# Optimization experiments

Measured on AMD Instinct MI355X. Metric: run time of the kernel, lower is better.

The kernel has to match this reference:

```python
import jax, jax.numpy as jnp
import numpy as np

D = 4096

def setup_inputs() -> dict:
    key = jax.random.key(0)
    ks = jax.random.split(key, 14)
    s = 1.0 / np.sqrt(D)
    return {
        "x": jax.random.normal(ks[0], (D,), jnp.float32),
        "state_xx": jax.random.normal(ks[1], (D,), jnp.float32),
        "aa": jax.random.normal(ks[2], (D,), jnp.float32),
        "bb": jax.random.uniform(ks[3], (D,), jnp.float32) + 0.5,  # positive running denom
        "pp": jax.random.normal(ks[4], (D,), jnp.float32),
        "w_key": jax.random.normal(ks[5], (D, D), jnp.float32) * s,
        "w_val": jax.random.normal(ks[6], (D, D), jnp.float32) * s,
        "w_rec": jax.random.normal(ks[7], (D, D), jnp.float32) * s,
        "w_out": jax.random.normal(ks[8], (D, D), jnp.float32) * s,
        "t_decay": -jax.random.uniform(ks[9], (D,), jnp.float32),  # module stores -exp(time_decay) < 0
        "t_first": jax.random.normal(ks[10], (D,), jnp.float32) * 0.5,
        "t_mix_k": jax.random.uniform(ks[11], (D,), jnp.float32),
        "t_mix_v": jax.random.uniform(ks[12], (D,), jnp.float32),
        "t_mix_r": jax.random.uniform(ks[13], (D,), jnp.float32),
    }


def reference(x, state_xx, aa, bb, pp, w_key, w_val, w_rec, w_out,
              t_decay, t_first, t_mix_k, t_mix_v, t_mix_r):
    # token mixing with previous token (state_xx)
    xk = x * t_mix_k + state_xx * (1.0 - t_mix_k)
    xv = x * t_mix_v + state_xx * (1.0 - t_mix_v)
    xr = x * t_mix_r + state_xx * (1.0 - t_mix_r)

    r = jax.nn.sigmoid(w_rec @ xr)
    k = w_key @ xk
    v = w_val @ xv

    # stabilized WKV output using current token bonus t_first
    ww = t_first + k
    p = jnp.maximum(pp, ww)
    e1 = jnp.exp(pp - p)
    e2 = jnp.exp(ww - p)
    a = e1 * aa + e2 * v
    b = e1 * bb + e2

    # stabilized state update with decay
    ww2 = pp + t_decay
    p2 = jnp.maximum(ww2, k)
    e1b = jnp.exp(ww2 - p2)
    e2b = jnp.exp(k - p2)
    new_aa = e1b * aa + e2b * v
    new_bb = e1b * bb + e2b
    new_pp = p2

    y = w_out @ (r * (a / b))
    # (output, new state_xx, new aa, new bb, new pp)
    return (y, x, new_aa, new_bb, new_pp)
```

## Files before the change

### kernel.cpp

```cpp
#include <hip/hip_runtime.h>

#define DIM 4096
#define BLK 256

__global__ void __launch_bounds__(BLK) vecprep_kernel(
    const float* __restrict__ x, const float* __restrict__ sxx,
    const float* __restrict__ tmk, const float* __restrict__ tmv,
    const float* __restrict__ tmr,
    float* __restrict__ xk, float* __restrict__ xv, float* __restrict__ xr) {
  int i = blockIdx.x * BLK + threadIdx.x;
  float xi = x[i], si = sxx[i];
  float mk = tmk[i], mv = tmv[i], mr = tmr[i];
  xk[i] = xi * mk + si * (1.0f - mk);
  xv[i] = xi * mv + si * (1.0f - mv);
  xr[i] = xi * mr + si * (1.0f - mr);
}

__global__ void __launch_bounds__(BLK) matvec3_kernel(
    const float* __restrict__ wr, const float* __restrict__ wk,
    const float* __restrict__ wv,
    const float* __restrict__ xr, const float* __restrict__ xk,
    const float* __restrict__ xv,
    float* __restrict__ rr, float* __restrict__ k, float* __restrict__ v) {
  const int row = blockIdx.x;
  const int t = threadIdx.x;
  const float4* wr4 = (const float4*)(wr + (size_t)row * DIM);
  const float4* wk4 = (const float4*)(wk + (size_t)row * DIM);
  const float4* wv4 = (const float4*)(wv + (size_t)row * DIM);
  const float4* xr4 = (const float4*)xr;
  const float4* xk4 = (const float4*)xk;
  const float4* xv4 = (const float4*)xv;
  float sr = 0.f, sk = 0.f, sv = 0.f;
#pragma unroll
  for (int j = 0; j < DIM / 4 / BLK; ++j) {
    int idx = t + j * BLK;
    float4 a = wr4[idx]; float4 b = xr4[idx];
    sr += a.x * b.x + a.y * b.y + a.z * b.z + a.w * b.w;
    float4 c = wk4[idx]; float4 d = xk4[idx];
    sk += c.x * d.x + c.y * d.y + c.z * d.z + c.w * d.w;
    float4 e = wv4[idx]; float4 f = xv4[idx];
    sv += e.x * f.x + e.y * f.y + e.z * f.z + e.w * f.w;
  }
  for (int off = 32; off > 0; off >>= 1) {
    sr += __shfl_down(sr, off);
    sk += __shfl_down(sk, off);
    sv += __shfl_down(sv, off);
  }
  __shared__ float red[4][3];
  int wave = t >> 6, lane = t & 63;
  if (lane == 0) { red[wave][0] = sr; red[wave][1] = sk; red[wave][2] = sv; }
  __syncthreads();
  if (t == 0) {
    float a = 0.f, b = 0.f, c = 0.f;
    for (int w = 0; w < 4; ++w) { a += red[w][0]; b += red[w][1]; c += red[w][2]; }
    rr[row] = a; k[row] = b; v[row] = c;
  }
}

__global__ void __launch_bounds__(BLK) wkv_kernel(
    const float* __restrict__ x, const float* __restrict__ aa,
    const float* __restrict__ bb, const float* __restrict__ pp,
    const float* __restrict__ t_decay, const float* __restrict__ t_first,
    const float* __restrict__ k, const float* __restrict__ v,
    const float* __restrict__ rr,
    float* __restrict__ rab, float* __restrict__ out_x,
    float* __restrict__ out_aa, float* __restrict__ out_bb,
    float* __restrict__ out_pp) {
  int i = blockIdx.x * BLK + threadIdx.x;
  float kk = k[i], vv = v[i];
  float r = 1.0f / (1.0f + expf(-rr[i]));
  float ppi = pp[i], aai = aa[i], bbi = bb[i];
  float ww = t_first[i] + kk;
  float p = fmaxf(ppi, ww);
  float e1 = expf(ppi - p), e2 = expf(ww - p);
  float a = e1 * aai + e2 * vv;
  float b = e1 * bbi + e2;
  rab[i] = r * (a / b);
  float ww2 = ppi + t_decay[i];
  float p2 = fmaxf(ww2, kk);
  float e1b = expf(ww2 - p2), e2b = expf(kk - p2);
  out_x[i] = x[i];
  out_aa[i] = e1b * aai + e2b * vv;
  out_bb[i] = e1b * bbi + e2b;
  out_pp[i] = p2;
}

__global__ void __launch_bounds__(BLK) matvec1_kernel(
    const float* __restrict__ w, const float* __restrict__ xin,
    float* __restrict__ y) {
  const int row = blockIdx.x;
  const int t = threadIdx.x;
  const float4* w4 = (const float4*)(w + (size_t)row * DIM);
  const float4* x4 = (const float4*)xin;
  float s = 0.f;
#pragma unroll
  for (int j = 0; j < DIM / 4 / BLK; ++j) {
    int idx = t + j * BLK;
    float4 a = w4[idx]; float4 b = x4[idx];
    s += a.x * b.x + a.y * b.y + a.z * b.z + a.w * b.w;
  }
  for (int off = 32; off > 0; off >>= 1) s += __shfl_down(s, off);
  __shared__ float red[4];
  int wave = t >> 6, lane = t & 63;
  if (lane == 0) red[wave] = s;
  __syncthreads();
  if (t == 0) y[row] = red[0] + red[1] + red[2] + red[3];
}

extern "C" void kernel_launch(void* const* d_in, const int* in_sizes, int n_in,
                              void* d_out, int out_size, void* d_ws, size_t ws_size,
                              hipStream_t stream) {
  const float* x       = (const float*)d_in[0];
  const float* sxx     = (const float*)d_in[1];
  const float* aa      = (const float*)d_in[2];
  const float* bb      = (const float*)d_in[3];
  const float* pp      = (const float*)d_in[4];
  const float* w_key   = (const float*)d_in[5];
  const float* w_val   = (const float*)d_in[6];
  const float* w_rec   = (const float*)d_in[7];
  const float* w_out   = (const float*)d_in[8];
  const float* t_decay = (const float*)d_in[9];
  const float* t_first = (const float*)d_in[10];
  const float* t_mix_k = (const float*)d_in[11];
  const float* t_mix_v = (const float*)d_in[12];
  const float* t_mix_r = (const float*)d_in[13];

  float* out    = (float*)d_out;
  float* y      = out;
  float* out_x  = out + DIM;
  float* out_aa = out + 2 * DIM;
  float* out_bb = out + 3 * DIM;
  float* out_pp = out + 4 * DIM;

  float* ws  = (float*)d_ws;
  float* xk  = ws;
  float* xv  = ws + DIM;
  float* xr  = ws + 2 * DIM;
  float* k   = ws + 3 * DIM;
  float* v   = ws + 4 * DIM;
  float* rr  = ws + 5 * DIM;
  float* rab = ws + 6 * DIM;

  vecprep_kernel<<<DIM / BLK, BLK, 0, stream>>>(x, sxx, t_mix_k, t_mix_v, t_mix_r,
                                                xk, xv, xr);
  matvec3_kernel<<<DIM, BLK, 0, stream>>>(w_rec, w_key, w_val, xr, xk, xv,
                                          rr, k, v);
  wkv_kernel<<<DIM / BLK, BLK, 0, stream>>>(x, aa, bb, pp, t_decay, t_first,
                                            k, v, rr, rab, out_x, out_aa,
                                            out_bb, out_pp);
  matvec1_kernel<<<DIM, BLK, 0, stream>>>(w_out, rab, y);
}
```

Baseline: 262.9 us.

## Fuse token mix and WKV into matvec, process four rows per block

Computes the token-mixed vectors inside the first matvec kernel and applies the WKV update in its epilogue, removing two kernel launches and the intermediate workspace traffic. Each block now processes four rows, so the input vector loads are reused across rows and more weight loads are in flight per thread. In exchange, each block recomputes the mixing of the full vector and register pressure goes up.

```diff
diff --git a/kernel.cpp b/kernel.cpp
--- a/kernel.cpp
+++ b/kernel.cpp
@@ -2,109 +2,152 @@
 
 #define DIM 4096
 #define BLK 256
+#define ROWS 4
 
-__global__ void __launch_bounds__(BLK) vecprep_kernel(
+__device__ __forceinline__ float dot4(float4 a, float4 b) {
+  return a.x * b.x + a.y * b.y + a.z * b.z + a.w * b.w;
+}
+
+__device__ __forceinline__ float4 mix4(float4 xi, float4 si, float4 m) {
+  float4 r;
+  r.x = fmaf(xi.x - si.x, m.x, si.x);
+  r.y = fmaf(xi.y - si.y, m.y, si.y);
+  r.z = fmaf(xi.z - si.z, m.z, si.z);
+  r.w = fmaf(xi.w - si.w, m.w, si.w);
+  return r;
+}
+
+__global__ void __launch_bounds__(BLK) fused3_kernel(
     const float* __restrict__ x, const float* __restrict__ sxx,
     const float* __restrict__ tmk, const float* __restrict__ tmv,
     const float* __restrict__ tmr,
-    float* __restrict__ xk, float* __restrict__ xv, float* __restrict__ xr) {
-  int i = blockIdx.x * BLK + threadIdx.x;
-  float xi = x[i], si = sxx[i];
-  float mk = tmk[i], mv = tmv[i], mr = tmr[i];
-  xk[i] = xi * mk + si * (1.0f - mk);
-  xv[i] = xi * mv + si * (1.0f - mv);
-  xr[i] = xi * mr + si * (1.0f - mr);
-}
-
-__global__ void __launch_bounds__(BLK) matvec3_kernel(
     const float* __restrict__ wr, const float* __restrict__ wk,
     const float* __restrict__ wv,
-    const float* __restrict__ xr, const float* __restrict__ xk,
-    const float* __restrict__ xv,
-    float* __restrict__ rr, float* __restrict__ k, float* __restrict__ v) {
-  const int row = blockIdx.x;
+    const float* __restrict__ aa, const float* __restrict__ bb,
+    const float* __restrict__ pp,
+    const float* __restrict__ t_decay, const float* __restrict__ t_first,
+    float* __restrict__ rab, float* __restrict__ out_x,
+    float* __restrict__ out_aa, float* __restrict__ out_bb,
+    float* __restrict__ out_pp) {
   const int t = threadIdx.x;
-  const float4* wr4 = (const float4*)(wr + (size_t)row * DIM);
-  const float4* wk4 = (const float4*)(wk + (size_t)row * DIM);
-  const float4* wv4 = (const float4*)(wv + (size_t)row * DIM);
-  const float4* xr4 = (const float4*)xr;
-  const float4* xk4 = (const float4*)xk;
-  const float4* xv4 = (const float4*)xv;
-  float sr = 0.f, sk = 0.f, sv = 0.f;
+  const int row0 = blockIdx.x * ROWS;
+
+  const float4* x4 = (const float4*)x;
+  const float4* s4 = (const float4*)sxx;
+  const float4* mk4 = (const float4*)tmk;
+  const float4* mv4 = (const float4*)tmv;
+  const float4* mr4 = (const float4*)tmr;
+
+  float4 fxr[4], fxk[4], fxv[4];
 #pragma unroll
-  for (int j = 0; j < DIM / 4 / BLK; ++j) {
+  for (int j = 0; j < 4; ++j) {
     int idx = t + j * BLK;
-    float4 a = wr4[idx]; float4 b = xr4[idx];
-    sr += a.x * b.x + a.y * b.y + a.z * b.z + a.w * b.w;
-    float4 c = wk4[idx]; float4 d = xk4[idx];
-    sk += c.x * d.x + c.y * d.y + c.z * d.z + c.w * d.w;
-    float4 e = wv4[idx]; float4 f = xv4[idx];
-    sv += e.x * f.x + e.y * f.y + e.z * f.z + e.w * f.w;
+    float4 xi = x4[idx], si = s4[idx];
+    fxk[j] = mix4(xi, si, mk4[idx]);
+    fxv[j] = mix4(xi, si, mv4[idx]);
+    fxr[j] = mix4(xi, si, mr4[idx]);
   }
+
+  float accr[ROWS], acck[ROWS], accv[ROWS];
+#pragma unroll
+  for (int r = 0; r < ROWS; ++r) { accr[r] = acck[r] = accv[r] = 0.f; }
+
+#pragma unroll
+  for (int r = 0; r < ROWS; ++r) {
+    const float4* wrp = (const float4*)(wr + (size_t)(row0 + r) * DIM);
+    const float4* wkp = (const float4*)(wk + (size_t)(row0 + r) * DIM);
+    const float4* wvp = (const float4*)(wv + (size_t)(row0 + r) * DIM);
+#pragma unroll
+    for (int j = 0; j < 4; ++j) {
+      int idx = t + j * BLK;
+      accr[r] += dot4(wrp[idx], fxr[j]);
+      acck[r] += dot4(wkp[idx], fxk[j]);
+      accv[r] += dot4(wvp[idx], fxv[j]);
+    }
+  }
+
+#pragma unroll
   for (int off = 32; off > 0; off >>= 1) {
-    sr += __shfl_down(sr, off);
-    sk += __shfl_down(sk, off);
-    sv += __shfl_down(sv, off);
+#pragma unroll
+    for (int r = 0; r < ROWS; ++r) {
+      accr[r] += __shfl_down(accr[r], off);
+      acck[r] += __shfl_down(acck[r], off);
+      accv[r] += __shfl_down(accv[r], off);
+    }
   }
-  __shared__ float red[4][3];
-  int wave = t >> 6, lane = t & 63;
-  if (lane == 0) { red[wave][0] = sr; red[wave][1] = sk; red[wave][2] = sv; }
+  __shared__ float red[4][ROWS * 3];
+  const int wave = t >> 6, lane = t & 63;
+  if (lane == 0) {
+#pragma unroll
+    for (int r = 0; r < ROWS; ++r) {
+      red[wave][r * 3 + 0] = accr[r];
+      red[wave][r * 3 + 1] = acck[r];
+      red[wave][r * 3 + 2] = accv[r];
+    }
+  }
   __syncthreads();
-  if (t == 0) {
-    float a = 0.f, b = 0.f, c = 0.f;
-    for (int w = 0; w < 4; ++w) { a += red[w][0]; b += red[w][1]; c += red[w][2]; }
-    rr[row] = a; k[row] = b; v[row] = c;
+
+  if (t < ROWS) {
+    const int row = row0 + t;
+    float sr = red[0][t * 3 + 0] + red[1][t * 3 + 0] + red[2][t * 3 + 0] + red[3][t * 3 + 0];
+    float sk = red[0][t * 3 + 1] + red[1][t * 3 + 1] + red[2][t * 3 + 1] + red[3][t * 3 + 1];
+    float sv = red[0][t * 3 + 2] + red[1][t * 3 + 2] + red[2][t * 3 + 2] + red[3][t * 3 + 2];
+
+    float rsig = 1.0f / (1.0f + expf(-sr));
+    float ppi = pp[row], aai = aa[row], bbi = bb[row];
+    float ww = t_first[row] + sk;
+    float p = fmaxf(ppi, ww);
+    float e1 = expf(ppi - p), e2 = expf(ww - p);
+    float a = e1 * aai + e2 * sv;
+    float b = e1 * bbi + e2;
+    rab[row] = rsig * (a / b);
+    float ww2 = ppi + t_decay[row];
+    float p2 = fmaxf(ww2, sk);
+    float e1b = expf(ww2 - p2), e2b = expf(sk - p2);
+    out_x[row]  = x[row];
+    out_aa[row] = e1b * aai + e2b * sv;
+    out_bb[row] = e1b * bbi + e2b;
+    out_pp[row] = p2;
   }
 }
 
-__global__ void __launch_bounds__(BLK) wkv_kernel(
-    const float* __restrict__ x, const float* __restrict__ aa,
-    const float* __restrict__ bb, const float* __restrict__ pp,
-    const float* __restrict__ t_decay, const float* __restrict__ t_first,
-    const float* __restrict__ k, const float* __restrict__ v,
-    const float* __restrict__ rr,
-    float* __restrict__ rab, float* __restrict__ out_x,
-    float* __restrict__ out_aa, float* __restrict__ out_bb,
-    float* __restrict__ out_pp) {
-  int i = blockIdx.x * BLK + threadIdx.x;
-  float kk = k[i], vv = v[i];
-  float r = 1.0f / (1.0f + expf(-rr[i]));
-  float ppi = pp[i], aai = aa[i], bbi = bb[i];
-  float ww = t_first[i] + kk;
-  float p = fmaxf(ppi, ww);
-  float e1 = expf(ppi - p), e2 = expf(ww - p);
-  float a = e1 * aai + e2 * vv;
-  float b = e1 * bbi + e2;
-  rab[i] = r * (a / b);
-  float ww2 = ppi + t_decay[i];
-  float p2 = fmaxf(ww2, kk);
-  float e1b = expf(ww2 - p2), e2b = expf(kk - p2);
-  out_x[i] = x[i];
-  out_aa[i] = e1b * aai + e2b * vv;
-  out_bb[i] = e1b * bbi + e2b;
-  out_pp[i] = p2;
-}
-
-__global__ void __launch_bounds__(BLK) matvec1_kernel(
+__global__ void __launch_bounds__(BLK) matvec_out_kernel(
     const float* __restrict__ w, const float* __restrict__ xin,
     float* __restrict__ y) {
-  const int row = blockIdx.x;
   const int t = threadIdx.x;
-  const float4* w4 = (const float4*)(w + (size_t)row * DIM);
+  const int row0 = blockIdx.x * ROWS;
   const float4* x4 = (const float4*)xin;
-  float s = 0.f;
+
+  float4 fx[4];
 #pragma unroll
-  for (int j = 0; j < DIM / 4 / BLK; ++j) {
-    int idx = t + j * BLK;
-    float4 a = w4[idx]; float4 b = x4[idx];
-    s += a.x * b.x + a.y * b.y + a.z * b.z + a.w * b.w;
+  for (int j = 0; j < 4; ++j) fx[j] = x4[t + j * BLK];
+
+  float acc[ROWS];
+#pragma unroll
+  for (int r = 0; r < ROWS; ++r) acc[r] = 0.f;
+
+#pragma unroll
+  for (int r = 0; r < ROWS; ++r) {
+    const float4* wp = (const float4*)(w + (size_t)(row0 + r) * DIM);
+#pragma unroll
+    for (int j = 0; j < 4; ++j) acc[r] += dot4(wp[t + j * BLK], fx[j]);
   }
-  for (int off = 32; off > 0; off >>= 1) s += __shfl_down(s, off);
-  __shared__ float red[4];
-  int wave = t >> 6, lane = t & 63;
-  if (lane == 0) red[wave] = s;
+
+#pragma unroll
+  for (int off = 32; off > 0; off >>= 1) {
+#pragma unroll
+    for (int r = 0; r < ROWS; ++r) acc[r] += __shfl_down(acc[r], off);
+  }
+  __shared__ float red[4][ROWS];
+  const int wave = t >> 6, lane = t & 63;
+  if (lane == 0) {
+#pragma unroll
+    for (int r = 0; r < ROWS; ++r) red[wave][r] = acc[r];
+  }
   __syncthreads();
-  if (t == 0) y[row] = red[0] + red[1] + red[2] + red[3];
+  if (t < ROWS) {
+    y[row0 + t] = red[0][t] + red[1][t] + red[2][t] + red[3][t];
+  }
 }
 
 extern "C" void kernel_launch(void* const* d_in, const int* in_sizes, int n_in,
@@ -132,21 +175,11 @@
   float* out_bb = out + 3 * DIM;
   float* out_pp = out + 4 * DIM;
 
-  float* ws  = (float*)d_ws;
-  float* xk  = ws;
-  float* xv  = ws + DIM;
-  float* xr  = ws + 2 * DIM;
-  float* k   = ws + 3 * DIM;
-  float* v   = ws + 4 * DIM;
-  float* rr  = ws + 5 * DIM;
-  float* rab = ws + 6 * DIM;
+  float* rab = (float*)d_ws;
 
-  vecprep_kernel<<<DIM / BLK, BLK, 0, stream>>>(x, sxx, t_mix_k, t_mix_v, t_mix_r,
-                                                xk, xv, xr);
-  matvec3_kernel<<<DIM, BLK, 0, stream>>>(w_rec, w_key, w_val, xr, xk, xv,
-                                          rr, k, v);
-  wkv_kernel<<<DIM / BLK, BLK, 0, stream>>>(x, aa, bb, pp, t_decay, t_first,
-                                            k, v, rr, rab, out_x, out_aa,
-                                            out_bb, out_pp);
-  matvec1_kernel<<<DIM, BLK, 0, stream>>>(w_out, rab, y);
+  fused3_kernel<<<DIM / ROWS, BLK, 0, stream>>>(
+      x, sxx, t_mix_k, t_mix_v, t_mix_r, w_rec, w_key, w_val,
+      aa, bb, pp, t_decay, t_first,
+      rab, out_x, out_aa, out_bb, out_pp);
+  matvec_out_kernel<<<DIM / ROWS, BLK, 0, stream>>>(w_out, rab, y);
 }
```

Result: no change. 258.9 us (-1.5%).

## Split matvec rows across waves with atomic accumulation and float4 prep

Applied to the files above, without the earlier changes.

Each matvec row is now split into four column chunks, each handled by one wave. A wave computes two rows, 2048 apart, and adds its partial sum to the output with atomicAdd, so block-level shared-memory reduction and __syncthreads are no longer needed. The prep kernel is vectorised to float4 and also zeroes the k, v, rr and y accumulators before the atomics run. The aim is to cut block reduction overhead and hold the x-vector slices in registers, at the cost of atomic traffic and summation order that is no longer deterministic.

```diff
diff --git a/kernel.cpp b/kernel.cpp
--- a/kernel.cpp
+++ b/kernel.cpp
@@ -3,57 +3,82 @@
 #define DIM 4096
 #define BLK 256
 
-__global__ void __launch_bounds__(BLK) vecprep_kernel(
+__device__ __forceinline__ float dot4(float4 a, float4 b) {
+  return a.x * b.x + a.y * b.y + a.z * b.z + a.w * b.w;
+}
+
+__device__ __forceinline__ float wave_reduce(float s) {
+#pragma unroll
+  for (int off = 32; off > 0; off >>= 1) s += __shfl_down(s, off);
+  return s;
+}
+
+__global__ void __launch_bounds__(BLK) prep_kernel(
     const float* __restrict__ x, const float* __restrict__ sxx,
     const float* __restrict__ tmk, const float* __restrict__ tmv,
     const float* __restrict__ tmr,
-    float* __restrict__ xk, float* __restrict__ xv, float* __restrict__ xr) {
+    float* __restrict__ xk, float* __restrict__ xv, float* __restrict__ xr,
+    float* __restrict__ k, float* __restrict__ v, float* __restrict__ rr,
+    float* __restrict__ y) {
   int i = blockIdx.x * BLK + threadIdx.x;
-  float xi = x[i], si = sxx[i];
-  float mk = tmk[i], mv = tmv[i], mr = tmr[i];
-  xk[i] = xi * mk + si * (1.0f - mk);
-  xv[i] = xi * mv + si * (1.0f - mv);
-  xr[i] = xi * mr + si * (1.0f - mr);
+  const float4* x4 = (const float4*)x;
+  const float4* s4 = (const float4*)sxx;
+  const float4* mk4 = (const float4*)tmk;
+  const float4* mv4 = (const float4*)tmv;
+  const float4* mr4 = (const float4*)tmr;
+  float4 xi = x4[i], si = s4[i];
+  float4 mk = mk4[i], mv = mv4[i], mr = mr4[i];
+  float4 ok, ov, orr;
+  ok.x = fmaf(xi.x - si.x, mk.x, si.x); ok.y = fmaf(xi.y - si.y, mk.y, si.y);
+  ok.z = fmaf(xi.z - si.z, mk.z, si.z); ok.w = fmaf(xi.w - si.w, mk.w, si.w);
+  ov.x = fmaf(xi.x - si.x, mv.x, si.x); ov.y = fmaf(xi.y - si.y, mv.y, si.y);
+  ov.z = fmaf(xi.z - si.z, mv.z, si.z); ov.w = fmaf(xi.w - si.w, mv.w, si.w);
+  orr.x = fmaf(xi.x - si.x, mr.x, si.x); orr.y = fmaf(xi.y - si.y, mr.y, si.y);
+  orr.z = fmaf(xi.z - si.z, mr.z, si.z); orr.w = fmaf(xi.w - si.w, mr.w, si.w);
+  ((float4*)xk)[i] = ok;
+  ((float4*)xv)[i] = ov;
+  ((float4*)xr)[i] = orr;
+  float4 z = make_float4(0.f, 0.f, 0.f, 0.f);
+  ((float4*)k)[i] = z;
+  ((float4*)v)[i] = z;
+  ((float4*)rr)[i] = z;
+  ((float4*)y)[i] = z;
 }
 
-__global__ void __launch_bounds__(BLK) matvec3_kernel(
+__global__ void __launch_bounds__(BLK) matvec3_split(
     const float* __restrict__ wr, const float* __restrict__ wk,
     const float* __restrict__ wv,
     const float* __restrict__ xr, const float* __restrict__ xk,
     const float* __restrict__ xv,
     float* __restrict__ rr, float* __restrict__ k, float* __restrict__ v) {
-  const int row = blockIdx.x;
-  const int t = threadIdx.x;
-  const float4* wr4 = (const float4*)(wr + (size_t)row * DIM);
-  const float4* wk4 = (const float4*)(wk + (size_t)row * DIM);
-  const float4* wv4 = (const float4*)(wv + (size_t)row * DIM);
-  const float4* xr4 = (const float4*)xr;
-  const float4* xk4 = (const float4*)xk;
-  const float4* xv4 = (const float4*)xv;
-  float sr = 0.f, sk = 0.f, sv = 0.f;
+  const int lane = threadIdx.x & 63;
+  const int wid = blockIdx.x * (BLK / 64) + (threadIdx.x >> 6);
+  const int c = wid & 3;
+  const int r0 = wid >> 2;
+  const int col = c * 256 + lane;
+
+  const float4* wmat[3] = {(const float4*)wr, (const float4*)wk, (const float4*)wv};
+  const float4* xvec[3] = {(const float4*)xr, (const float4*)xk, (const float4*)xv};
+  float* ovec[3] = {rr, k, v};
+
 #pragma unroll
-  for (int j = 0; j < DIM / 4 / BLK; ++j) {
-    int idx = t + j * BLK;
-    float4 a = wr4[idx]; float4 b = xr4[idx];
-    sr += a.x * b.x + a.y * b.y + a.z * b.z + a.w * b.w;
-    float4 c = wk4[idx]; float4 d = xk4[idx];
-    sk += c.x * d.x + c.y * d.y + c.z * d.z + c.w * d.w;
-    float4 e = wv4[idx]; float4 f = xv4[idx];
-    sv += e.x * f.x + e.y * f.y + e.z * f.z + e.w * f.w;
-  }
-  for (int off = 32; off > 0; off >>= 1) {
-    sr += __shfl_down(sr, off);
-    sk += __shfl_down(sk, off);
-    sv += __shfl_down(sv, off);
-  }
-  __shared__ float red[4][3];
-  int wave = t >> 6, lane = t & 63;
-  if (lane == 0) { red[wave][0] = sr; red[wave][1] = sk; red[wave][2] = sv; }
-  __syncthreads();
-  if (t == 0) {
-    float a = 0.f, b = 0.f, c = 0.f;
-    for (int w = 0; w < 4; ++w) { a += red[w][0]; b += red[w][1]; c += red[w][2]; }
-    rr[row] = a; k[row] = b; v[row] = c;
+  for (int m = 0; m < 3; ++m) {
+    const float4* xp = xvec[m];
+    float4 xf0 = xp[col];
+    float4 xf1 = xp[col + 64];
+    float4 xf2 = xp[col + 128];
+    float4 xf3 = xp[col + 192];
+#pragma unroll
+    for (int h = 0; h < 2; ++h) {
+      const int r = r0 + h * 2048;
+      const float4* wrow = wmat[m] + (size_t)r * 1024 + col;
+      float s = dot4(wrow[0], xf0);
+      s += dot4(wrow[64], xf1);
+      s += dot4(wrow[128], xf2);
+      s += dot4(wrow[192], xf3);
+      s = wave_reduce(s);
+      if (lane == 0) atomicAdd(ovec[m] + r, s);
+    }
   }
 }
 
@@ -85,26 +110,31 @@
   out_pp[i] = p2;
 }
 
-__global__ void __launch_bounds__(BLK) matvec1_kernel(
+__global__ void __launch_bounds__(BLK) matvec_out_split(
     const float* __restrict__ w, const float* __restrict__ xin,
     float* __restrict__ y) {
-  const int row = blockIdx.x;
-  const int t = threadIdx.x;
-  const float4* w4 = (const float4*)(w + (size_t)row * DIM);
-  const float4* x4 = (const float4*)xin;
-  float s = 0.f;
+  const int lane = threadIdx.x & 63;
+  const int wid = blockIdx.x * (BLK / 64) + (threadIdx.x >> 6);
+  const int c = wid & 3;
+  const int r0 = wid >> 2;
+  const int col = c * 256 + lane;
+
+  const float4* xp = (const float4*)xin;
+  float4 xf0 = xp[col];
+  float4 xf1 = xp[col + 64];
+  float4 xf2 = xp[col + 128];
+  float4 xf3 = xp[col + 192];
 #pragma unroll
-  for (int j = 0; j < DIM / 4 / BLK; ++j) {
-    int idx = t + j * BLK;
-    float4 a = w4[idx]; float4 b = x4[idx];
-    s += a.x * b.x + a.y * b.y + a.z * b.z + a.w * b.w;
+  for (int h = 0; h < 2; ++h) {
+    const int r = r0 + h * 2048;
+    const float4* wrow = (const float4*)w + (size_t)r * 1024 + col;
+    float s = dot4(wrow[0], xf0);
+    s += dot4(wrow[64], xf1);
+    s += dot4(wrow[128], xf2);
+    s += dot4(wrow[192], xf3);
+    s = wave_reduce(s);
+    if (lane == 0) atomicAdd(y + r, s);
   }
-  for (int off = 32; off > 0; off >>= 1) s += __shfl_down(s, off);
-  __shared__ float red[4];
-  int wave = t >> 6, lane = t & 63;
-  if (lane == 0) red[wave] = s;
-  __syncthreads();
-  if (t == 0) y[row] = red[0] + red[1] + red[2] + red[3];
 }
 
 extern "C" void kernel_launch(void* const* d_in, const int* in_sizes, int n_in,
@@ -141,12 +171,12 @@
   float* rr  = ws + 5 * DIM;
   float* rab = ws + 6 * DIM;
 
-  vecprep_kernel<<<DIM / BLK, BLK, 0, stream>>>(x, sxx, t_mix_k, t_mix_v, t_mix_r,
-                                                xk, xv, xr);
-  matvec3_kernel<<<DIM, BLK, 0, stream>>>(w_rec, w_key, w_val, xr, xk, xv,
+  prep_kernel<<<DIM / 4 / BLK, BLK, 0, stream>>>(
+      x, sxx, t_mix_k, t_mix_v, t_mix_r, xk, xv, xr, k, v, rr, y);
+  matvec3_split<<<2048, BLK, 0, stream>>>(w_rec, w_key, w_val, xr, xk, xv,
                                           rr, k, v);
   wkv_kernel<<<DIM / BLK, BLK, 0, stream>>>(x, aa, bb, pp, t_decay, t_first,
                                             k, v, rr, rab, out_x, out_aa,
                                             out_bb, out_pp);
-  matvec1_kernel<<<DIM, BLK, 0, stream>>>(w_out, rab, y);
+  matvec_out_split<<<2048, BLK, 0, stream>>>(w_out, rab, y);
 }
```

Measured after the change: 260.7 us. About the same (-0.8%).

## Fuse token-mix into matvec, use wave-per-row blocks with shared input vector

Applied to the files above, without the earlier changes.

The separate vecprep kernel is removed, and each block of the three-matrix matvec now computes its mixed input vector into shared memory directly. Both matvec kernels switch from one 256-thread block per row to 8 rows per block, with each wave handling two rows using float4 loads and a wave-only reduction. Block indices are swizzled to spread matrices and row groups across the grid. This is meant to cut launch count, block-level reduction sync and the workspace round trip. In exchange, each block redundantly recomputes the full 4096-element mix, and register pressure rises from holding the input vector in registers.

```diff
diff --git a/kernel.cpp b/kernel.cpp
--- a/kernel.cpp
+++ b/kernel.cpp
@@ -1,59 +1,79 @@
 #include <hip/hip_runtime.h>
 
 #define DIM 4096
+#define F4  1024
 #define BLK 256
+#define RPB 8
+#define NB3 (3 * DIM / RPB)
+#define NBO (DIM / RPB)
 
-__global__ void __launch_bounds__(BLK) vecprep_kernel(
+__device__ __forceinline__ float dot4(float4 a, float4 b) {
+  return a.x * b.x + a.y * b.y + a.z * b.z + a.w * b.w;
+}
+
+__device__ __forceinline__ float wave_reduce(float s) {
+#pragma unroll
+  for (int off = 32; off > 0; off >>= 1) s += __shfl_down(s, off);
+  return s;
+}
+
+__device__ __forceinline__ float4 mix4(float4 xi, float4 si, float4 m) {
+  float4 r;
+  r.x = fmaf(xi.x - si.x, m.x, si.x);
+  r.y = fmaf(xi.y - si.y, m.y, si.y);
+  r.z = fmaf(xi.z - si.z, m.z, si.z);
+  r.w = fmaf(xi.w - si.w, m.w, si.w);
+  return r;
+}
+
+__global__ void __launch_bounds__(BLK) matvec3_rows(
     const float* __restrict__ x, const float* __restrict__ sxx,
     const float* __restrict__ tmk, const float* __restrict__ tmv,
     const float* __restrict__ tmr,
-    float* __restrict__ xk, float* __restrict__ xv, float* __restrict__ xr) {
-  int i = blockIdx.x * BLK + threadIdx.x;
-  float xi = x[i], si = sxx[i];
-  float mk = tmk[i], mv = tmv[i], mr = tmr[i];
-  xk[i] = xi * mk + si * (1.0f - mk);
-  xv[i] = xi * mv + si * (1.0f - mv);
-  xr[i] = xi * mr + si * (1.0f - mr);
-}
-
-__global__ void __launch_bounds__(BLK) matvec3_kernel(
     const float* __restrict__ wr, const float* __restrict__ wk,
     const float* __restrict__ wv,
-    const float* __restrict__ xr, const float* __restrict__ xk,
-    const float* __restrict__ xv,
-    float* __restrict__ rr, float* __restrict__ k, float* __restrict__ v) {
-  const int row = blockIdx.x;
+    float* __restrict__ o_rr, float* __restrict__ o_k, float* __restrict__ o_v) {
+  __shared__ float4 xs[F4];
   const int t = threadIdx.x;
-  const float4* wr4 = (const float4*)(wr + (size_t)row * DIM);
-  const float4* wk4 = (const float4*)(wk + (size_t)row * DIM);
-  const float4* wv4 = (const float4*)(wv + (size_t)row * DIM);
-  const float4* xr4 = (const float4*)xr;
-  const float4* xk4 = (const float4*)xk;
-  const float4* xv4 = (const float4*)xv;
-  float sr = 0.f, sk = 0.f, sv = 0.f;
+  const int b = (blockIdx.x & 7) * (NB3 / 8) + (blockIdx.x >> 3);
+  const int m = b / (DIM / RPB);
+  const int rg = b % (DIM / RPB);
+
+  const float* mixv = (m == 0) ? tmr : (m == 1) ? tmk : tmv;
+  const float4* w4 = (const float4*)((m == 0) ? wr : (m == 1) ? wk : wv);
+  float* out = (m == 0) ? o_rr : (m == 1) ? o_k : o_v;
+
+  const float4* x4 = (const float4*)x;
+  const float4* s4 = (const float4*)sxx;
+  const float4* m4 = (const float4*)mixv;
 #pragma unroll
-  for (int j = 0; j < DIM / 4 / BLK; ++j) {
-    int idx = t + j * BLK;
-    float4 a = wr4[idx]; float4 b = xr4[idx];
-    sr += a.x * b.x + a.y * b.y + a.z * b.z + a.w * b.w;
-    float4 c = wk4[idx]; float4 d = xk4[idx];
-    sk += c.x * d.x + c.y * d.y + c.z * d.z + c.w * d.w;
-    float4 e = wv4[idx]; float4 f = xv4[idx];
-    sv += e.x * f.x + e.y * f.y + e.z * f.z + e.w * f.w;
+  for (int p = 0; p < 4; ++p) {
+    int i = t + p * BLK;
+    xs[i] = mix4(x4[i], s4[i], m4[i]);
   }
-  for (int off = 32; off > 0; off >>= 1) {
-    sr += __shfl_down(sr, off);
-    sk += __shfl_down(sk, off);
-    sv += __shfl_down(sv, off);
-  }
-  __shared__ float red[4][3];
-  int wave = t >> 6, lane = t & 63;
-  if (lane == 0) { red[wave][0] = sr; red[wave][1] = sk; red[wave][2] = sv; }
   __syncthreads();
-  if (t == 0) {
-    float a = 0.f, b = 0.f, c = 0.f;
-    for (int w = 0; w < 4; ++w) { a += red[w][0]; b += red[w][1]; c += red[w][2]; }
-    rr[row] = a; k[row] = b; v[row] = c;
+
+  const int wave = t >> 6, lane = t & 63;
+  float4 xf[16];
+#pragma unroll
+  for (int j = 0; j < 16; ++j) xf[j] = xs[j * 64 + lane];
+
+#pragma unroll
+  for (int rr2 = 0; rr2 < 2; ++rr2) {
+    const int row = rg * RPB + wave * 2 + rr2;
+    const float4* wp = w4 + (size_t)row * F4 + lane;
+    float acc = 0.f;
+    float4 wbuf[8];
+#pragma unroll
+    for (int j = 0; j < 8; ++j) wbuf[j] = wp[j * 64];
+#pragma unroll
+    for (int j = 0; j < 8; ++j) acc += dot4(wbuf[j], xf[j]);
+#pragma unroll
+    for (int j = 0; j < 8; ++j) wbuf[j] = wp[(8 + j) * 64];
+#pragma unroll
+    for (int j = 0; j < 8; ++j) acc += dot4(wbuf[j], xf[8 + j]);
+    acc = wave_reduce(acc);
+    if (lane == 0) out[row] = acc;
   }
 }
 
@@ -85,26 +105,45 @@
   out_pp[i] = p2;
 }
 
-__global__ void __launch_bounds__(BLK) matvec1_kernel(
+__global__ void __launch_bounds__(BLK) matvec_out_rows(
     const float* __restrict__ w, const float* __restrict__ xin,
     float* __restrict__ y) {
-  const int row = blockIdx.x;
+  __shared__ float4 xs[F4];
   const int t = threadIdx.x;
-  const float4* w4 = (const float4*)(w + (size_t)row * DIM);
+  const int b = (blockIdx.x & 7) * (NBO / 8) + (blockIdx.x >> 3);
+  const int rg = b;
+
   const float4* x4 = (const float4*)xin;
-  float s = 0.f;
 #pragma unroll
-  for (int j = 0; j < DIM / 4 / BLK; ++j) {
-    int idx = t + j * BLK;
-    float4 a = w4[idx]; float4 b = x4[idx];
-    s += a.x * b.x + a.y * b.y + a.z * b.z + a.w * b.w;
+  for (int p = 0; p < 4; ++p) {
+    int i = t + p * BLK;
+    xs[i] = x4[i];
   }
-  for (int off = 32; off > 0; off >>= 1) s += __shfl_down(s, off);
-  __shared__ float red[4];
-  int wave = t >> 6, lane = t & 63;
-  if (lane == 0) red[wave] = s;
   __syncthreads();
-  if (t == 0) y[row] = red[0] + red[1] + red[2] + red[3];
+
+  const int wave = t >> 6, lane = t & 63;
+  float4 xf[16];
+#pragma unroll
+  for (int j = 0; j < 16; ++j) xf[j] = xs[j * 64 + lane];
+
+  const float4* w4 = (const float4*)w;
+#pragma unroll
+  for (int rr2 = 0; rr2 < 2; ++rr2) {
+    const int row = rg * RPB + wave * 2 + rr2;
+    const float4* wp = w4 + (size_t)row * F4 + lane;
+    float acc = 0.f;
+    float4 wbuf[8];
+#pragma unroll
+    for (int j = 0; j < 8; ++j) wbuf[j] = wp[j * 64];
+#pragma unroll
+    for (int j = 0; j < 8; ++j) acc += dot4(wbuf[j], xf[j]);
+#pragma unroll
+    for (int j = 0; j < 8; ++j) wbuf[j] = wp[(8 + j) * 64];
+#pragma unroll
+    for (int j = 0; j < 8; ++j) acc += dot4(wbuf[j], xf[8 + j]);
+    acc = wave_reduce(acc);
+    if (lane == 0) y[row] = acc;
+  }
 }
 
 extern "C" void kernel_launch(void* const* d_in, const int* in_sizes, int n_in,
@@ -133,20 +172,15 @@
   float* out_pp = out + 4 * DIM;
 
   float* ws  = (float*)d_ws;
-  float* xk  = ws;
-  float* xv  = ws + DIM;
-  float* xr  = ws + 2 * DIM;
-  float* k   = ws + 3 * DIM;
-  float* v   = ws + 4 * DIM;
-  float* rr  = ws + 5 * DIM;
-  float* rab = ws + 6 * DIM;
+  float* k   = ws;
+  float* v   = ws + DIM;
+  float* rr  = ws + 2 * DIM;
+  float* rab = ws + 3 * DIM;
 
-  vecprep_kernel<<<DIM / BLK, BLK, 0, stream>>>(x, sxx, t_mix_k, t_mix_v, t_mix_r,
-                                                xk, xv, xr);
-  matvec3_kernel<<<DIM, BLK, 0, stream>>>(w_rec, w_key, w_val, xr, xk, xv,
-                                          rr, k, v);
+  matvec3_rows<<<NB3, BLK, 0, stream>>>(x, sxx, t_mix_k, t_mix_v, t_mix_r,
+                                        w_rec, w_key, w_val, rr, k, v);
   wkv_kernel<<<DIM / BLK, BLK, 0, stream>>>(x, aa, bb, pp, t_decay, t_first,
                                             k, v, rr, rab, out_x, out_aa,
                                             out_bb, out_pp);
-  matvec1_kernel<<<DIM, BLK, 0, stream>>>(w_out, rab, y);
+  matvec_out_rows<<<NBO, BLK, 0, stream>>>(w_out, rab, y);
 }
```

Result: no change. 262.0 us (-0.3%).
